# Kernel optimization log

Hardware: AMD Instinct MI355X
Metric: run time of the kernel (lower is better)

The kernel has to match this reference:

```python
import jax, jax.numpy as jnp
import numpy as np

EPS = 1e-5      # BatchNorm eps (eval mode, running_mean=0, running_var=1)
SLOPE = 0.2     # LeakyReLU negative slope


def knn_idx(x, k):
    # x: (B, C, N) -> indices of k nearest neighbors (B, N, k)
    xx = jnp.sum(x * x, axis=1)                      # (B, N)
    inner = jnp.einsum('bcn,bcm->bnm', x, x)         # (B, N, N)
    pd = 2.0 * inner - xx[:, :, None] - xx[:, None, :]  # -squared distance
    return jax.lax.top_k(pd, k)[1]


def edge_feature(x, k):
    # x: (B, C, N) -> (B, N, k, 2C) edge features [x_j - x_i, x_i]
    B, C, N = x.shape
    idx = knn_idx(x, k)                              # (B, N, k)
    xt = jnp.transpose(x, (0, 2, 1))                 # (B, N, C)
    feat = jax.vmap(lambda t, i: t[i])(xt, idx)      # (B, N, k, C)
    center = xt[:, :, None, :]                       # (B, N, 1, C)
    return jnp.concatenate(
        [feat - center, jnp.broadcast_to(center, (B, N, k, C))], axis=-1)


def conv_bn_lrelu_max(e, W, g, b):
    # e: (B, N, k, Cin), W: (O, Cin) 1x1 conv; BN eval (mean=0, var=1); max over k
    h = jnp.einsum('bnkc,oc->bnko', e, W)
    scale = g / jnp.sqrt(1.0 + EPS)
    h = h * scale + b
    h = jnp.where(h >= 0, h, SLOPE * h)
    return jnp.transpose(jnp.max(h, axis=2), (0, 2, 1))  # (B, O, N)


def setup_inputs() -> dict:
    key = jax.random.key(0)
    ks = jax.random.split(key, 17)
    B, N, k = 8, 2048, 20
    x = jax.random.normal(ks[0], (B, 3, N), dtype=jnp.float32)
    def w(kk, o, c):
        return jax.random.normal(kk, (o, c), dtype=jnp.float32) * (1.0 / np.sqrt(c))
    W1 = w(ks[1], 64, 6)
    W2 = w(ks[2], 64, 128)
    W3 = w(ks[3], 128, 128)
    W4 = w(ks[4], 256, 256)
    W5 = w(ks[5], 1024, 512)
    def gb(kk, c):
        k1, k2 = jax.random.split(kk)
        g = 0.5 + jax.random.uniform(k1, (c,), dtype=jnp.float32)
        b = 0.1 * jax.random.normal(k2, (c,), dtype=jnp.float32)
        return g, b
    g1, b1 = gb(ks[6], 64)
    g2, b2 = gb(ks[7], 64)
    g3, b3 = gb(ks[8], 128)
    g4, b4 = gb(ks[9], 256)
    g5, b5 = gb(ks[10], 1024)
    return {"x": x, "W1": W1, "W2": W2, "W3": W3, "W4": W4, "W5": W5,
            "g1": g1, "b1": b1, "g2": g2, "b2": b2, "g3": g3, "b3": b3,
            "g4": g4, "b4": b4, "g5": g5, "b5": b5, "k": k}


def reference(x, W1, W2, W3, W4, W5, g1, b1, g2, b2, g3, b3, g4, b4, g5, b5, k):
    h1 = conv_bn_lrelu_max(edge_feature(x, k), W1, g1, b1)    # (B, 64, N)
    h2 = conv_bn_lrelu_max(edge_feature(h1, k), W2, g2, b2)   # (B, 64, N)
    h3 = conv_bn_lrelu_max(edge_feature(h2, k), W3, g3, b3)   # (B, 128, N)
    h4 = conv_bn_lrelu_max(edge_feature(h3, k), W4, g4, b4)   # (B, 256, N)
    cat = jnp.concatenate([h1, h2, h3, h4], axis=1)           # (B, 512, N)
    h = jnp.einsum('bcn,oc->bon', cat, W5)                    # (B, 1024, N)
    h = h * (g5 / jnp.sqrt(1.0 + EPS))[:, None] + b5[:, None]
    h = jnp.where(h >= 0, h, SLOPE * h)
    return jnp.max(h, axis=-1)                                # (B, 1024) maxpool=True
```

## Files before the change

### kernel.cpp

```cpp
#include <hip/hip_runtime.h>
#include <math.h>

#define BB 8
#define NN 2048
#define KK 20

static __device__ __forceinline__ float lrelu(float h) {
    return h >= 0.f ? h : 0.2f * h;
}

__global__ __launch_bounds__(256) void transpose_x(const float* __restrict__ x,
                                                   float* __restrict__ xt) {
    int t = blockIdx.x * 256 + threadIdx.x;
    if (t >= BB * NN) return;
    int b = t / NN, n = t % NN;
    const float* xb = x + (size_t)b * 3 * NN;
    float4 v;
    v.x = xb[n];
    v.y = xb[NN + n];
    v.z = xb[2 * NN + n];
    v.w = 0.f;
    reinterpret_cast<float4*>(xt)[t] = v;
}

__global__ __launch_bounds__(256) void xx_kernel(const float* __restrict__ F, int stride, int off,
                                                 int C, float* __restrict__ xx) {
    int t = blockIdx.x * 256 + threadIdx.x;
    if (t >= BB * NN) return;
    const float* p = F + (size_t)t * stride + off;
    float s = 0.f;
    for (int c = 0; c < C; ++c) { float v = p[c]; s += v * v; }
    xx[t] = s;
}

template <int C>
__global__ __launch_bounds__(256, 4) void knn_kernel(const float* __restrict__ F, int stride,
                                                     int off, const float* __restrict__ xx,
                                                     unsigned long long* __restrict__ part) {
    constexpr int ROWS = 32, TM = 64, NSPLIT = 4, MSPAN = NN / NSPLIT;
    constexpr int CK = (C >= 64) ? 32 : 4;
    constexpr int SK = (C >= 64) ? 36 : 4;
    constexpr int NKT = (C + CK - 1) / CK;
    constexpr int S4 = SK / 4;
    constexpr int C4 = CK / 4;
    constexpr int PDS = TM + 8;

    __shared__ __align__(16) float As[ROWS * SK];
    __shared__ __align__(16) float Bs[TM * SK];
    __shared__ __align__(16) float pdb[ROWS * PDS];
    __shared__ float xxA[ROWS];
    __shared__ float xxB[TM];

    const int t = threadIdx.x;
    const int split = blockIdx.x & (NSPLIT - 1);
    const int rg = (blockIdx.x >> 2) & 63;
    const int b = blockIdx.x >> 8;
    const int n0 = rg * ROWS;
    const float* Fb = F + (size_t)b * NN * stride + off;
    const float* xxb = xx + (size_t)b * NN;

    unsigned long long tv[KK];
#pragma unroll
    for (int i = 0; i < KK; ++i) tv[i] = 0ull;

    const int rl = t & 3;
    const int cl = t >> 2;
    const int rr = t >> 3;
    const int sub = t & 7;

    if (t < ROWS) xxA[t] = xxb[n0 + t];

    for (int mt = 0; mt < MSPAN / TM; ++mt) {
        const int m0 = split * MSPAN + mt * TM;
        float acc[8];
#pragma unroll
        for (int j = 0; j < 8; ++j) acc[j] = 0.f;

        for (int kt = 0; kt < NKT; ++kt) {
            __syncthreads();
            if constexpr (C >= 64) {
                float4* As4w = reinterpret_cast<float4*>(As);
                float4* Bs4w = reinterpret_cast<float4*>(Bs);
                for (int i = t; i < ROWS * S4; i += 256) {
                    int r = i / S4, c4i = i % S4;
                    float4 v = make_float4(0.f, 0.f, 0.f, 0.f);
                    if (c4i < C4)
                        v = *reinterpret_cast<const float4*>(
                            Fb + (size_t)(n0 + r) * stride + kt * CK + 4 * c4i);
                    As4w[i] = v;
                }
                for (int i = t; i < TM * S4; i += 256) {
                    int r = i / S4, c4i = i % S4;
                    float4 v = make_float4(0.f, 0.f, 0.f, 0.f);
                    if (c4i < C4)
                        v = *reinterpret_cast<const float4*>(
                            Fb + (size_t)(m0 + r) * stride + kt * CK + 4 * c4i);
                    Bs4w[i] = v;
                }
            } else {
                if (t < ROWS)
                    reinterpret_cast<float4*>(As)[t] =
                        *reinterpret_cast<const float4*>(Fb + (size_t)(n0 + t) * 4);
                if (t < TM)
                    reinterpret_cast<float4*>(Bs)[t] =
                        *reinterpret_cast<const float4*>(Fb + (size_t)(m0 + t) * 4);
            }
            if (kt == 0 && t < TM) xxB[t] = xxb[m0 + t];
            __syncthreads();

            const float4* As4 = reinterpret_cast<const float4*>(As);
            const float4* Bs4 = reinterpret_cast<const float4*>(Bs);
#pragma unroll
            for (int c4 = 0; c4 < C4; ++c4) {
                float4 b0 = Bs4[cl * S4 + c4];
#pragma unroll
                for (int j = 0; j < 8; ++j) {
                    float4 a = As4[(rl + 4 * j) * S4 + c4];
                    acc[j] += a.x * b0.x;
                    acc[j] += a.y * b0.y;
                    acc[j] += a.z * b0.z;
                    acc[j] += a.w * b0.w;
                }
            }
        }
#pragma unroll
        for (int j = 0; j < 8; ++j) {
            int r = rl + 4 * j;
            pdb[r * PDS + cl] = (2.f * acc[j] - xxA[r]) - xxB[cl];
        }
        __syncthreads();

        unsigned long long kc[8];
#pragma unroll
        for (int jj = 0; jj < 8; ++jj) {
            int ml = sub + 8 * jj;
            float v = pdb[rr * PDS + ml];
            unsigned int u = __float_as_uint(v);
            unsigned int sv = u ^ (unsigned int)(((int)u >> 31) | 0x80000000);
            kc[jj] = ((unsigned long long)sv << 32) | (unsigned int)(~(m0 + ml));
        }
#pragma unroll
        for (int jj = 0; jj < 8; ++jj) {
            if (kc[jj] > tv[KK - 1]) {
                unsigned long long c = kc[jj];
#pragma unroll
                for (int s = KK - 1; s >= 1; --s) {
                    bool shs = c > tv[s];
                    bool shp = c > tv[s - 1];
                    unsigned long long tmp = shp ? tv[s - 1] : c;
                    tv[s] = shs ? tmp : tv[s];
                }
                tv[0] = (c > tv[0]) ? c : tv[0];
            }
        }
    }

    unsigned long long* op =
        part + (((size_t)b * NN + n0 + rr) * NSPLIT + split) * KK;
    for (int s = 0; s < KK; ++s) {
        unsigned long long m = tv[0];
#pragma unroll
        for (int d = 1; d < 8; d <<= 1) {
            unsigned long long o = __shfl_xor(m, d);
            m = (o > m) ? o : m;
        }
        if (sub == 0) op[s] = m;
        bool win = (tv[0] == m);
#pragma unroll
        for (int q = 0; q < KK - 1; ++q) tv[q] = win ? tv[q + 1] : tv[q];
        tv[KK - 1] = win ? 0ull : tv[KK - 1];
    }
}

__global__ __launch_bounds__(256) void knn_merge(const unsigned long long* __restrict__ part,
                                                 int* __restrict__ idxOut) {
    int t = blockIdx.x * 256 + threadIdx.x;
    int q = t & 3, row = t >> 2;
    if (row >= BB * NN) return;
    unsigned long long k[KK];
    const unsigned long long* lp = part + ((size_t)row * 4 + q) * KK;
#pragma unroll
    for (int s = 0; s < KK; ++s) k[s] = lp[s];
    int* op = idxOut + (size_t)row * KK;
    for (int s = 0; s < KK; ++s) {
        unsigned long long m = k[0];
        unsigned long long o1 = __shfl_xor(m, 1);
        m = (o1 > m) ? o1 : m;
        unsigned long long o2 = __shfl_xor(m, 2);
        m = (o2 > m) ? o2 : m;
        if (q == 0) op[s] = (int)(~(unsigned int)m);
        bool win = (k[0] == m);
#pragma unroll
        for (int qq = 0; qq < KK - 1; ++qq) k[qq] = win ? k[qq + 1] : k[qq];
        k[KK - 1] = win ? 0ull : k[KK - 1];
    }
}

__global__ __launch_bounds__(256) void gemm_yz(const float* __restrict__ F, int stride, int off,
                                               const float* __restrict__ W, int K, int O,
                                               float* __restrict__ out) {
    __shared__ float As[128 * 36];
    __shared__ float Ws[128 * 36];
    const int t = threadIdx.x;
    const int row0 = blockIdx.x * 128;
    const int col0 = blockIdx.y * 128;
    const int OC = 2 * O;
    float acc[8][8];
#pragma unroll
    for (int i = 0; i < 8; ++i)
#pragma unroll
        for (int j = 0; j < 8; ++j) acc[i][j] = 0.f;

    for (int kt = 0; kt < K; kt += 32) {
        __syncthreads();
        for (int i = t; i < 128 * 32; i += 256) {
            int r = i >> 5, c = i & 31;
            int k = kt + c;
            As[r * 36 + c] = (k < K) ? F[(size_t)(row0 + r) * stride + off + k] : 0.f;
            float wv = 0.f;
            if (k < K) {
                int o2 = col0 + r;
                if (o2 < O) wv = W[(size_t)o2 * 2 * K + k];
                else wv = W[(size_t)(o2 - O) * 2 * K + K + k] - W[(size_t)(o2 - O) * 2 * K + k];
            }
            Ws[r * 36 + c] = wv;
        }
        __syncthreads();
        const int r0 = t & 15, c0 = t >> 4;
        const float4* As4 = reinterpret_cast<const float4*>(As);
        const float4* Ws4 = reinterpret_cast<const float4*>(Ws);
#pragma unroll
        for (int k4 = 0; k4 < 8; ++k4) {
            float4 a[8], w[8];
#pragma unroll
            for (int i = 0; i < 8; ++i) a[i] = As4[(r0 + 16 * i) * 9 + k4];
#pragma unroll
            for (int j = 0; j < 8; ++j) w[j] = Ws4[(c0 + 16 * j) * 9 + k4];
#pragma unroll
            for (int i = 0; i < 8; ++i)
#pragma unroll
                for (int j = 0; j < 8; ++j) {
                    acc[i][j] += a[i].x * w[j].x;
                    acc[i][j] += a[i].y * w[j].y;
                    acc[i][j] += a[i].z * w[j].z;
                    acc[i][j] += a[i].w * w[j].w;
                }
        }
    }
    const int r0 = t & 15, c0 = t >> 4;
#pragma unroll
    for (int i = 0; i < 8; ++i)
#pragma unroll
        for (int j = 0; j < 8; ++j)
            out[(size_t)(row0 + r0 + 16 * i) * OC + col0 + c0 + 16 * j] = acc[i][j];
}

__global__ __launch_bounds__(256) void neighbor_max(const float* __restrict__ yz,
                                                    const int* __restrict__ idx,
                                                    const float* __restrict__ g,
                                                    const float* __restrict__ bia, int O,
                                                    int outOff, float* __restrict__ cat) {
    int t = blockIdx.x * 256 + threadIdx.x;
    int og = O >> 2;
    if (t >= BB * NN * og) return;
    int o4 = t % og;
    int pn = t / og;
    int bbase = (pn >> 11) << 11;
    const int* ip = idx + (size_t)pn * KK;
    int O2 = O * 2;
    float mx = -INFINITY, my = -INFINITY, mz = -INFINITY, mw = -INFINITY;
    for (int j = 0; j < KK; ++j) {
        int nb = ip[j];
        const float4 v =
            *reinterpret_cast<const float4*>(yz + (size_t)(bbase + nb) * O2 + (o4 << 2));
        mx = fmaxf(mx, v.x); my = fmaxf(my, v.y); mz = fmaxf(mz, v.z); mw = fmaxf(mw, v.w);
    }
    const float4 z = *reinterpret_cast<const float4*>(yz + (size_t)pn * O2 + O + (o4 << 2));
    int o = o4 << 2;
    const float inv = 1.f / sqrtf(1.f + 1e-5f);
    float4 r;
    r.x = lrelu((mx + z.x) * (g[o + 0] * inv) + bia[o + 0]);
    r.y = lrelu((my + z.y) * (g[o + 1] * inv) + bia[o + 1]);
    r.z = lrelu((mz + z.z) * (g[o + 2] * inv) + bia[o + 2]);
    r.w = lrelu((mw + z.w) * (g[o + 3] * inv) + bia[o + 3]);
    *reinterpret_cast<float4*>(cat + (size_t)pn * 512 + outOff + o) = r;
}

__global__ __launch_bounds__(256) void final_gemm_max(const float* __restrict__ A,
                                                      const float* __restrict__ W,
                                                      const float* __restrict__ g,
                                                      const float* __restrict__ bia,
                                                      float* __restrict__ partial) {
    __shared__ float As[128 * 36];
    __shared__ float Ws[128 * 36];
    __shared__ float red[16 * 132];
    const int t = threadIdx.x;
    const int row0 = blockIdx.x * 128;
    const int col0 = blockIdx.y * 128;
    float acc[8][8];
#pragma unroll
    for (int i = 0; i < 8; ++i)
#pragma unroll
        for (int j = 0; j < 8; ++j) acc[i][j] = 0.f;

    for (int kt = 0; kt < 512; kt += 32) {
        __syncthreads();
        for (int i = t; i < 128 * 32; i += 256) {
            int r = i >> 5, c = i & 31;
            int k = kt + c;
            As[r * 36 + c] = A[(size_t)(row0 + r) * 512 + k];
            Ws[r * 36 + c] = W[(size_t)(col0 + r) * 512 + k];
        }
        __syncthreads();
        const int r0 = t & 15, c0 = t >> 4;
        const float4* As4 = reinterpret_cast<const float4*>(As);
        const float4* Ws4 = reinterpret_cast<const float4*>(Ws);
#pragma unroll
        for (int k4 = 0; k4 < 8; ++k4) {
            float4 a[8], w[8];
#pragma unroll
            for (int i = 0; i < 8; ++i) a[i] = As4[(r0 + 16 * i) * 9 + k4];
#pragma unroll
            for (int j = 0; j < 8; ++j) w[j] = Ws4[(c0 + 16 * j) * 9 + k4];
#pragma unroll
            for (int i = 0; i < 8; ++i)
#pragma unroll
                for (int j = 0; j < 8; ++j) {
                    acc[i][j] += a[i].x * w[j].x;
                    acc[i][j] += a[i].y * w[j].y;
                    acc[i][j] += a[i].z * w[j].z;
                    acc[i][j] += a[i].w * w[j].w;
                }
        }
    }
    const int r0 = t & 15, c0 = t >> 4;
    const float inv = 1.f / sqrtf(1.f + 1e-5f);
#pragma unroll
    for (int j = 0; j < 8; ++j) {
        int o = col0 + c0 + 16 * j;
        float s = g[o] * inv;
        float bb = bia[o];
        float cm = -INFINITY;
#pragma unroll
        for (int i = 0; i < 8; ++i) {
            float h = acc[i][j] * s + bb;
            h = lrelu(h);
            cm = fmaxf(cm, h);
        }
        red[r0 * 132 + c0 + 16 * j] = cm;
    }
    __syncthreads();
    if (t < 128) {
        float m = -INFINITY;
        for (int q = 0; q < 16; ++q) m = fmaxf(m, red[q * 132 + t]);
        partial[(size_t)blockIdx.x * 1024 + col0 + t] = m;
    }
}

__global__ __launch_bounds__(256) void final_reduce(const float* __restrict__ partial,
                                                    float* __restrict__ out) {
    int t = blockIdx.x * 256 + threadIdx.x;
    if (t >= BB * 1024) return;
    int b = t >> 10, o = t & 1023;
    float m = -INFINITY;
    for (int q = 0; q < 16; ++q) m = fmaxf(m, partial[(size_t)(b * 16 + q) * 1024 + o]);
    out[t] = m;
}

extern "C" void kernel_launch(void* const* d_in, const int* in_sizes, int n_in, void* d_out,
                              int out_size, void* d_ws, size_t ws_size, hipStream_t stream) {
    const float* x  = (const float*)d_in[0];
    const float* W1 = (const float*)d_in[1];
    const float* W2 = (const float*)d_in[2];
    const float* W3 = (const float*)d_in[3];
    const float* W4 = (const float*)d_in[4];
    const float* W5 = (const float*)d_in[5];
    const float* g1 = (const float*)d_in[6];  const float* b1 = (const float*)d_in[7];
    const float* g2 = (const float*)d_in[8];  const float* b2 = (const float*)d_in[9];
    const float* g3 = (const float*)d_in[10]; const float* b3 = (const float*)d_in[11];
    const float* g4 = (const float*)d_in[12]; const float* b4 = (const float*)d_in[13];
    const float* g5 = (const float*)d_in[14]; const float* b5 = (const float*)d_in[15];

    float* ws   = (float*)d_ws;
    float* xt   = ws;
    float* cat  = xt + 65536;
    float* yz   = cat + 8388608;
    float* xxb  = yz + 8388608;
    int*   idxb = (int*)(xxb + 16384);
    float* part = (float*)(idxb + 327680);
    unsigned long long* knnp = (unsigned long long*)yz;

    dim3 blk(256);

    transpose_x<<<dim3(64), blk, 0, stream>>>(x, xt);

    xx_kernel<<<dim3(64), blk, 0, stream>>>(xt, 4, 0, 3, xxb);
    knn_kernel<3><<<dim3(2048), blk, 0, stream>>>(xt, 4, 0, xxb, knnp);
    knn_merge<<<dim3(256), blk, 0, stream>>>(knnp, idxb);
    gemm_yz<<<dim3(128, 1), blk, 0, stream>>>(xt, 4, 0, W1, 3, 64, yz);
    neighbor_max<<<dim3(1024), blk, 0, stream>>>(yz, idxb, g1, b1, 64, 0, cat);

    xx_kernel<<<dim3(64), blk, 0, stream>>>(cat, 512, 0, 64, xxb);
    knn_kernel<64><<<dim3(2048), blk, 0, stream>>>(cat, 512, 0, xxb, knnp);
    knn_merge<<<dim3(256), blk, 0, stream>>>(knnp, idxb);
    gemm_yz<<<dim3(128, 1), blk, 0, stream>>>(cat, 512, 0, W2, 64, 64, yz);
    neighbor_max<<<dim3(1024), blk, 0, stream>>>(yz, idxb, g2, b2, 64, 64, cat);

    xx_kernel<<<dim3(64), blk, 0, stream>>>(cat, 512, 64, 64, xxb);
    knn_kernel<64><<<dim3(2048), blk, 0, stream>>>(cat, 512, 64, xxb, knnp);
    knn_merge<<<dim3(256), blk, 0, stream>>>(knnp, idxb);
    gemm_yz<<<dim3(128, 2), blk, 0, stream>>>(cat, 512, 64, W3, 64, 128, yz);
    neighbor_max<<<dim3(2048), blk, 0, stream>>>(yz, idxb, g3, b3, 128, 128, cat);

    xx_kernel<<<dim3(64), blk, 0, stream>>>(cat, 512, 128, 128, xxb);
    knn_kernel<128><<<dim3(2048), blk, 0, stream>>>(cat, 512, 128, xxb, knnp);
    knn_merge<<<dim3(256), blk, 0, stream>>>(knnp, idxb);
    gemm_yz<<<dim3(128, 4), blk, 0, stream>>>(cat, 512, 128, W4, 128, 256, yz);
    neighbor_max<<<dim3(4096), blk, 0, stream>>>(yz, idxb, g4, b4, 256, 256, cat);

    final_gemm_max<<<dim3(128, 8), blk, 0, stream>>>(cat, W5, g5, b5, part);
    final_reduce<<<dim3(32), blk, 0, stream>>>(part, (float*)d_out);
}
```

Measured before the change: 1.499 ms.

## Filter kNN candidates with per-row threshold queue and halve column splits

Replaces the dense pdb staging and full per-thread insertion scan with a per-row threshold filter. Candidates are pushed into a shared queue via LDS atomics only if they beat the row's current 20th-best, and that threshold is refreshed after each tile by a shuffle reduction. The column split drops from 4 to 2, giving each block a longer span so the threshold prunes more, and knn_merge is changed to merge 2 partial lists. Costs are LDS atomics and ballot-driven loops, plus half as many blocks, which lowers parallelism.

After: 1.418 ms, median of 2. 1.06x faster.

```diff
diff --git a/kernel.cpp b/kernel.cpp
--- a/kernel.cpp
+++ b/kernel.cpp
@@ -37,24 +37,26 @@
 __global__ __launch_bounds__(256, 4) void knn_kernel(const float* __restrict__ F, int stride,
                                                      int off, const float* __restrict__ xx,
                                                      unsigned long long* __restrict__ part) {
-    constexpr int ROWS = 32, TM = 64, NSPLIT = 4, MSPAN = NN / NSPLIT;
+    constexpr int ROWS = 32, TM = 64, NSPLIT = 2, MSPAN = NN / NSPLIT;
     constexpr int CK = (C >= 64) ? 32 : 4;
     constexpr int SK = (C >= 64) ? 36 : 4;
     constexpr int NKT = (C + CK - 1) / CK;
     constexpr int S4 = SK / 4;
     constexpr int C4 = CK / 4;
-    constexpr int PDS = TM + 8;
+    constexpr int QS = 66;
 
     __shared__ __align__(16) float As[ROWS * SK];
     __shared__ __align__(16) float Bs[TM * SK];
-    __shared__ __align__(16) float pdb[ROWS * PDS];
     __shared__ float xxA[ROWS];
     __shared__ float xxB[TM];
+    __shared__ __align__(16) unsigned long long qbuf[ROWS * QS];
+    __shared__ unsigned int qcnt[ROWS];
+    __shared__ unsigned long long thr[ROWS];
 
     const int t = threadIdx.x;
     const int split = blockIdx.x & (NSPLIT - 1);
-    const int rg = (blockIdx.x >> 2) & 63;
-    const int b = blockIdx.x >> 8;
+    const int rg = (blockIdx.x >> 1) & 63;
+    const int b = blockIdx.x >> 7;
     const int n0 = rg * ROWS;
     const float* Fb = F + (size_t)b * NN * stride + off;
     const float* xxb = xx + (size_t)b * NN;
@@ -68,7 +70,11 @@
     const int rr = t >> 3;
     const int sub = t & 7;
 
-    if (t < ROWS) xxA[t] = xxb[n0 + t];
+    if (t < ROWS) {
+        xxA[t] = xxb[n0 + t];
+        thr[t] = 0ull;
+        qcnt[t] = 0u;
+    }
 
     for (int mt = 0; mt < MSPAN / TM; ++mt) {
         const int m0 = split * MSPAN + mt * TM;
@@ -123,34 +129,52 @@
                 }
             }
         }
+
 #pragma unroll
         for (int j = 0; j < 8; ++j) {
             int r = rl + 4 * j;
-            pdb[r * PDS + cl] = (2.f * acc[j] - xxA[r]) - xxB[cl];
-        }
-        __syncthreads();
-
-        unsigned long long kc[8];
-#pragma unroll
-        for (int jj = 0; jj < 8; ++jj) {
-            int ml = sub + 8 * jj;
-            float v = pdb[rr * PDS + ml];
+            float v = (2.f * acc[j] - xxA[r]) - xxB[cl];
             unsigned int u = __float_as_uint(v);
             unsigned int sv = u ^ (unsigned int)(((int)u >> 31) | 0x80000000);
-            kc[jj] = ((unsigned long long)sv << 32) | (unsigned int)(~(m0 + ml));
-        }
-#pragma unroll
-        for (int jj = 0; jj < 8; ++jj) {
-            if (kc[jj] > tv[KK - 1]) {
-                unsigned long long c = kc[jj];
-#pragma unroll
-                for (int s = KK - 1; s >= 1; --s) {
-                    bool shs = c > tv[s];
-                    bool shp = c > tv[s - 1];
-                    unsigned long long tmp = shp ? tv[s - 1] : c;
-                    tv[s] = shs ? tmp : tv[s];
-                }
-                tv[0] = (c > tv[0]) ? c : tv[0];
+            unsigned long long kc = ((unsigned long long)sv << 32) | (unsigned int)(~(m0 + cl));
+            unsigned long long th = thr[r];
+            if (th == 0ull) {
+                qbuf[r * QS + cl] = kc;
+            } else if (kc > th) {
+                unsigned int pos = atomicAdd(&qcnt[r], 1u);
+                qbuf[r * QS + pos] = kc;
+            }
+        }
+        __syncthreads();
+
+        {
+            unsigned long long throw_ = thr[rr];
+            int n = (throw_ == 0ull) ? TM : (int)qcnt[rr];
+            for (int s = 0; s < TM / 8; ++s) {
+                int qi = s * 8 + sub;
+                bool act = qi < n;
+                if (__ballot(act) == 0ull) break;
+                unsigned long long c = act ? qbuf[rr * QS + qi] : 0ull;
+                if (c > tv[KK - 1]) {
+#pragma unroll
+                    for (int sl = KK - 1; sl >= 1; --sl) {
+                        bool shs = c > tv[sl];
+                        bool shp = c > tv[sl - 1];
+                        unsigned long long tmp = shp ? tv[sl - 1] : c;
+                        tv[sl] = shs ? tmp : tv[sl];
+                    }
+                    tv[0] = (c > tv[0]) ? c : tv[0];
+                }
+            }
+            unsigned long long m19 = tv[KK - 1];
+#pragma unroll
+            for (int d = 1; d < 8; d <<= 1) {
+                unsigned long long o = __shfl_xor(m19, d);
+                m19 = (o > m19) ? o : m19;
+            }
+            if (sub == 0) {
+                thr[rr] = m19;
+                qcnt[rr] = 0u;
             }
         }
     }
@@ -175,10 +199,10 @@
 __global__ __launch_bounds__(256) void knn_merge(const unsigned long long* __restrict__ part,
                                                  int* __restrict__ idxOut) {
     int t = blockIdx.x * 256 + threadIdx.x;
-    int q = t & 3, row = t >> 2;
+    int q = t & 1, row = t >> 1;
     if (row >= BB * NN) return;
     unsigned long long k[KK];
-    const unsigned long long* lp = part + ((size_t)row * 4 + q) * KK;
+    const unsigned long long* lp = part + ((size_t)row * 2 + q) * KK;
 #pragma unroll
     for (int s = 0; s < KK; ++s) k[s] = lp[s];
     int* op = idxOut + (size_t)row * KK;
@@ -186,8 +210,6 @@
         unsigned long long m = k[0];
         unsigned long long o1 = __shfl_xor(m, 1);
         m = (o1 > m) ? o1 : m;
-        unsigned long long o2 = __shfl_xor(m, 2);
-        m = (o2 > m) ? o2 : m;
         if (q == 0) op[s] = (int)(~(unsigned int)m);
         bool win = (k[0] == m);
 #pragma unroll
@@ -395,26 +417,26 @@
     transpose_x<<<dim3(64), blk, 0, stream>>>(x, xt);
 
     xx_kernel<<<dim3(64), blk, 0, stream>>>(xt, 4, 0, 3, xxb);
-    knn_kernel<3><<<dim3(2048), blk, 0, stream>>>(xt, 4, 0, xxb, knnp);
-    knn_merge<<<dim3(256), blk, 0, stream>>>(knnp, idxb);
+    knn_kernel<3><<<dim3(1024), blk, 0, stream>>>(xt, 4, 0, xxb, knnp);
+    knn_merge<<<dim3(128), blk, 0, stream>>>(knnp, idxb);
     gemm_yz<<<dim3(128, 1), blk, 0, stream>>>(xt, 4, 0, W1, 3, 64, yz);
     neighbor_max<<<dim3(1024), blk, 0, stream>>>(yz, idxb, g1, b1, 64, 0, cat);
 
     xx_kernel<<<dim3(64), blk, 0, stream>>>(cat, 512, 0, 64, xxb);
-    knn_kernel<64><<<dim3(2048), blk, 0, stream>>>(cat, 512, 0, xxb, knnp);
-    knn_merge<<<dim3(256), blk, 0, stream>>>(knnp, idxb);
+    knn_kernel<64><<<dim3(1024), blk, 0, stream>>>(cat, 512, 0, xxb, knnp);
+    knn_merge<<<dim3(128), blk, 0, stream>>>(knnp, idxb);
     gemm_yz<<<dim3(128, 1), blk, 0, stream>>>(cat, 512, 0, W2, 64, 64, yz);
     neighbor_max<<<dim3(1024), blk, 0, stream>>>(yz, idxb, g2, b2, 64, 64, cat);
 
     xx_kernel<<<dim3(64), blk, 0, stream>>>(cat, 512, 64, 64, xxb);
-    knn_kernel<64><<<dim3(2048), blk, 0, stream>>>(cat, 512, 64, xxb, knnp);
-    knn_merge<<<dim3(256), blk, 0, stream>>>(knnp, idxb);
+    knn_kernel<64><<<dim3(1024), blk, 0, stream>>>(cat, 512, 64, xxb, knnp);
+    knn_merge<<<dim3(128), blk, 0, stream>>>(knnp, idxb);
     gemm_yz<<<dim3(128, 2), blk, 0, stream>>>(cat, 512, 64, W3, 64, 128, yz);
     neighbor_max<<<dim3(2048), blk, 0, stream>>>(yz, idxb, g3, b3, 128, 128, cat);
 
     xx_kernel<<<dim3(64), blk, 0, stream>>>(cat, 512, 128, 128, xxb);
-    knn_kernel<128><<<dim3(2048), blk, 0, stream>>>(cat, 512, 128, xxb, knnp);
-    knn_merge<<<dim3(256), blk, 0, stream>>>(knnp, idxb);
+    knn_kernel<128><<<dim3(1024), blk, 0, stream>>>(cat, 512, 128, xxb, knnp);
+    knn_merge<<<dim3(128), blk, 0, stream>>>(knnp, idxb);
     gemm_yz<<<dim3(128, 4), blk, 0, stream>>>(cat, 512, 128, W4, 128, 256, yz);
     neighbor_max<<<dim3(4096), blk, 0, stream>>>(yz, idxb, g4, b4, 256, 256, cat);
 
```
